# Optimization experiments

Measured on AMD Instinct MI355X. Metric: run time of the kernel, lower is better.

The kernel has to match this reference:

```python
import jax, jax.numpy as jnp
import numpy as np

D_MODEL = 512
D_ALPHA = 100
D_PH = 80
SCALE = 1.0 / np.sqrt(D_MODEL)


def gru_cell(x, h, Wih, Whh, bih, bhh):
    # PyTorch GRU gate order: r, z, n
    gi = x @ Wih.T + bih
    gh = h @ Whh.T + bhh
    ir, iz, inn = jnp.split(gi, 3, axis=-1)
    hr, hz, hn = jnp.split(gh, 3, axis=-1)
    r = jax.nn.sigmoid(ir + hr)
    z = jax.nn.sigmoid(iz + hz)
    n = jnp.tanh(inn + r * hn)
    return (1.0 - z) * n + z * h


def attend(q, k, v):
    # q: [B,D], k/v: [B,L,D]
    scores = jnp.einsum('bd,bld->bl', q, k) * SCALE
    a = jax.nn.softmax(scores, axis=-1)  # [B,L]
    o = jnp.einsum('bl,bld->bd', a, v)
    return a, o


def setup_inputs() -> dict:
    key = jax.random.key(0)
    ks = jax.random.split(key, 25)
    D = D_MODEL

    def u(k, shape, fan):
        return jax.random.uniform(k, shape, jnp.float32, -1.0, 1.0) / np.sqrt(fan)

    inp = {
        'text': jax.random.randint(ks[0], (256, 128), 0, D_ALPHA),
        'tgt': jax.random.randint(ks[1], (256, 64), 0, D_PH),
        'E_alpha': jax.random.normal(ks[2], (D_ALPHA, D), jnp.float32),
        'enc_Wih_f': u(ks[3], (3 * D, D), D),
        'enc_Whh_f': u(ks[4], (3 * D, D), D),
        'enc_bih_f': u(ks[5], (3 * D,), D),
        'enc_bhh_f': u(ks[6], (3 * D,), D),
        'enc_Wih_b': u(ks[7], (3 * D, D), D),
        'enc_Whh_b': u(ks[8], (3 * D, D), D),
        'enc_bih_b': u(ks[9], (3 * D,), D),
        'enc_bhh_b': u(ks[10], (3 * D,), D),
        'hpost_W': u(ks[11], (D, 2 * D), 2 * D),
        'hpost_b': u(ks[12], (D,), 2 * D),
        'wk_W': u(ks[13], (D, 2 * D), 2 * D),
        'wk_b': u(ks[14], (D,), 2 * D),
        'wv_W': u(ks[15], (D, 2 * D), 2 * D),
        'wv_b': u(ks[16], (D,), 2 * D),
        'E_ph': jax.random.normal(ks[17], (D_PH, D), jnp.float32),
        'dec_Wih': u(ks[18], (3 * D, 2 * D), 2 * D),
        'dec_Whh': u(ks[19], (3 * D, D), D),
        'dec_bih': u(ks[20], (3 * D,), D),
        'dec_bhh': u(ks[21], (3 * D,), D),
        'post_W': u(ks[22], (D_PH, D), D),
        'post_b': u(ks[23], (D_PH,), D),
    }
    return inp


def reference(text, tgt, E_alpha, enc_Wih_f, enc_Whh_f, enc_bih_f, enc_bhh_f,
              enc_Wih_b, enc_Whh_b, enc_bih_b, enc_bhh_b, hpost_W, hpost_b,
              wk_W, wk_b, wv_W, wv_b, E_ph, dec_Wih, dec_Whh, dec_bih,
              dec_bhh, post_W, post_b):
    B, LT = text.shape
    LP = tgt.shape[1]

    # ---- Encoder: bidirectional single-layer GRU (eval: dropout = identity)
    emb = E_alpha[text]                     # [B,LT,D]
    xs = jnp.swapaxes(emb, 0, 1)            # [LT,B,D]
    h0 = jnp.zeros((B, D_MODEL), emb.dtype)

    def mk_step(Wih, Whh, bih, bhh):
        def step(h, x):
            h2 = gru_cell(x, h, Wih, Whh, bih, bhh)
            return h2, h2
        return step

    hF, ysF = jax.lax.scan(mk_step(enc_Wih_f, enc_Whh_f, enc_bih_f, enc_bhh_f), h0, xs)
    hB, ysB = jax.lax.scan(mk_step(enc_Wih_b, enc_Whh_b, enc_bih_b, enc_bhh_b), h0, xs[::-1])
    ysB = ysB[::-1]
    enc_o = jnp.swapaxes(jnp.concatenate([ysF, ysB], axis=-1), 0, 1)  # [B,LT,2D]
    h = jnp.tanh(jnp.concatenate([hF, hB], axis=-1) @ hpost_W.T + hpost_b)  # [B,D]

    k = enc_o @ wk_W.T + wk_b               # [B,LT,D]
    v = enc_o @ wv_W.T + wv_b               # [B,LT,D]

    # ---- initial attention from encoder hidden; eval-mode first token is argmax
    # over tgt[:,0] reshaped to [B,1,1], i.e. always index 0.
    a_sl0, a_o0 = attend(h, k, v)
    dec_i0 = jnp.zeros((B,), jnp.int32)

    def dstep(carry, _):
        hh, a_o, a_sl, dec_i = carry
        e = E_ph[dec_i]                                  # [B,D]
        x = gru_cell(jnp.concatenate([e, a_o], axis=-1), hh,
                     dec_Wih, dec_Whh, dec_bih, dec_bhh)  # [B,D]
        o = x @ post_W.T + post_b                         # [B,D_PH]
        n_sl, n_o = attend(x, k, v)
        nxt = jnp.argmax(o, axis=-1).astype(jnp.int32)
        return (x, n_o, n_sl, nxt), (a_sl, o)

    _, (attn_t, res_t) = jax.lax.scan(dstep, (h, a_o0, a_sl0, dec_i0), None, length=LP)
    attn = jnp.swapaxes(attn_t, 0, 1)        # [B,LP,LT]
    res = jnp.swapaxes(res_t, 0, 1)          # [B,LP,D_PH]
    return attn, res
```

## Files before the change

### kernel.cpp

```cpp
#include <hip/hip_runtime.h>
#include <math.h>

#define B   256
#define LT  128
#define LP  64
#define DM  512
#define D3  1536
#define DPH 80
#define SCALE_F 0.044194173824159216f

__device__ __forceinline__ float dot4(float4 a, float4 b) {
    return a.x*b.x + a.y*b.y + a.z*b.z + a.w*b.w;
}
__device__ __forceinline__ float sigmoidf_(float x) {
    return 1.0f / (1.0f + expf(-x));
}

__device__ __forceinline__ void group_barrier(int* cnt, int target) {
    __syncthreads();
    if (threadIdx.x == 0) {
        __hip_atomic_fetch_add(cnt, 1, __ATOMIC_RELEASE,
                               __HIP_MEMORY_SCOPE_AGENT);
        while (__hip_atomic_load(cnt, __ATOMIC_RELAXED,
                                 __HIP_MEMORY_SCOPE_AGENT) < target)
            __builtin_amdgcn_s_sleep(16);
        __builtin_amdgcn_fence(__ATOMIC_ACQUIRE, "agent");
    }
    __syncthreads();
}

__global__ __launch_bounds__(256) void precompG_kernel(
    const float* __restrict__ Emb, const float* __restrict__ W,
    const float* __restrict__ bias, float* __restrict__ G,
    int wstride, int woff)
{
    const int n  = blockIdx.x * 256 + threadIdx.x;
    const int r0 = blockIdx.y * 4;
    __shared__ float es[4][DM];
    for (int i = threadIdx.x; i < 4 * DM; i += 256)
        es[i >> 9][i & 511] = Emb[(r0 + (i >> 9)) * DM + (i & 511)];
    __syncthreads();
    float acc[4] = {0.f, 0.f, 0.f, 0.f};
    const float* wr = &W[(size_t)n * wstride + woff];
    for (int j = 0; j < DM; j += 4) {
        float4 w4 = *(const float4*)&wr[j];
        #pragma unroll
        for (int rr = 0; rr < 4; ++rr) {
            float4 e4 = *(const float4*)&es[rr][j];
            acc[rr] += dot4(e4, w4);
        }
    }
    float bv = bias[n];
    #pragma unroll
    for (int rr = 0; rr < 4; ++rr)
        G[(r0 + rr) * D3 + n] = acc[rr] + bv;
}

__global__ __launch_bounds__(512, 1) void enc_persist_kernel(
    const float* __restrict__ Gf, const float* __restrict__ Gb,
    const float* __restrict__ Whh_f, const float* __restrict__ Whh_b,
    const float* __restrict__ bhh_f, const float* __restrict__ bhh_b,
    const int* __restrict__ text,
    float* __restrict__ hF0, float* __restrict__ hF1,
    float* __restrict__ hB0, float* __restrict__ hB1,
    float* __restrict__ E,
    const float* __restrict__ hpost_W, const float* __restrict__ hpost_b,
    float* __restrict__ hd0, int* __restrict__ bar)
{
    __shared__ float Wl[48][516];
    __shared__ float As[2][64][36];
    __shared__ float xs[1024];
    __shared__ float bl[48];

    const int tid  = threadIdx.x;
    const int blk  = blockIdx.x;
    const int dir  = blk & 1;
    const int bblk = (blk >> 1) & 3;
    const int jblk = blk >> 3;
    const int jtile = jblk * 16;
    const int btile = bblk * 64;
    int* cnt = bar + (blk & 7);

    const float* G   = dir ? Gb : Gf;
    const float* Whh = dir ? Whh_b : Whh_f;
    const float* bhh = dir ? bhh_b : bhh_f;
    float* h0 = dir ? hB0 : hF0;
    float* h1 = dir ? hB1 : hF1;
    const int yoff = dir ? DM : 0;

    for (int i = tid; i < 48 * 128; i += 512) {
        const int r = i >> 7, c = (i & 127) << 2;
        *(float4*)&Wl[r][c] =
            *(const float4*)&Whh[(size_t)((r >> 4) * DM + jtile + (r & 15)) * DM + c];
    }
    if (tid < 48) bl[tid] = bhh[(tid >> 4) * DM + jtile + (tid & 15)];
    __syncthreads();

    const int jj   = tid & 15;
    const int rg   = tid >> 4;
    const int lrow = tid >> 3;
    const int lcol = (tid & 7) * 4;

    for (int s = 0; s < LT; ++s) {
        const int t = dir ? (LT - 1 - s) : s;
        const float* hin = (s & 1) ? h1 : h0;
        float* hout      = (s & 1) ? h0 : h1;

        float acc[2][3];
        #pragma unroll
        for (int m = 0; m < 2; ++m) {
            acc[m][0] = 0.f; acc[m][1] = 0.f; acc[m][2] = 0.f;
        }

        float4 rA = *(const float4*)&hin[(btile + lrow) * DM + lcol];
        int buf = 0;
        for (int kc = 0; kc < 16; ++kc) {
            *(float4*)&As[buf][lrow][lcol] = rA;
            __syncthreads();
            if (kc < 15)
                rA = *(const float4*)&hin[(btile + lrow) * DM + (kc + 1) * 32 + lcol];
            const int kb = kc * 32;
            #pragma unroll
            for (int c4 = 0; c4 < 8; ++c4) {
                float4 bv0 = *(float4*)&Wl[jj][kb + c4 * 4];
                float4 bv1 = *(float4*)&Wl[16 + jj][kb + c4 * 4];
                float4 bv2 = *(float4*)&Wl[32 + jj][kb + c4 * 4];
                #pragma unroll
                for (int m = 0; m < 2; ++m) {
                    float4 av = *(float4*)&As[buf][rg * 2 + m][c4 * 4];
                    acc[m][0] += dot4(av, bv0);
                    acc[m][1] += dot4(av, bv1);
                    acc[m][2] += dot4(av, bv2);
                }
            }
            buf ^= 1;
            __syncthreads();
        }

        const int j = jtile + jj;
        #pragma unroll
        for (int m = 0; m < 2; ++m) {
            const int b = btile + rg * 2 + m;
            const int c = text[b * LT + t];
            float hr = acc[m][0] + bl[jj];
            float hz = acc[m][1] + bl[16 + jj];
            float hn = acc[m][2] + bl[32 + jj];
            float r = sigmoidf_(G[c * D3 + j] + hr);
            float z = sigmoidf_(G[c * D3 + DM + j] + hz);
            float n = tanhf(G[c * D3 + 2 * DM + j] + r * hn);
            float hp = hin[b * DM + j];
            float hv = (1.f - z) * n + z * hp;
            hout[b * DM + j] = hv;
            E[(size_t)(b * LT + t) * 1024 + yoff + j] = hv;
        }
        if (s < LT - 1) group_barrier(cnt, 32 * (s + 1));
    }

    group_barrier(bar + 8, 256);
    {
        const int b = blk;
        for (int i = tid; i < 1024; i += 512) {
            xs[i] = (i < DM) ? hF0[b * DM + i] : hB0[b * DM + (i - DM)];
        }
        __syncthreads();
        if (tid < DM) {
            const float* wr = &hpost_W[tid * 1024];
            float acc = 0.f;
            for (int jx = 0; jx < 1024; jx += 4)
                acc += dot4(*(const float4*)&xs[jx], *(const float4*)&wr[jx]);
            hd0[b * DM + tid] = tanhf(acc + hpost_b[tid]);
        }
    }
}

__global__ __launch_bounds__(256) void kv_chunk_kernel(
    const float* __restrict__ E,
    const float* __restrict__ wk, const float* __restrict__ wv,
    const float* __restrict__ kb, const float* __restrict__ vb,
    float* __restrict__ T, int r0)
{
    __shared__ float As[64][36];
    __shared__ float Bk[64][36];
    __shared__ float Bv[64][36];
    const int tid = threadIdx.x;
    const int nn = tid & 15, bb = tid >> 4;
    const int ntile = blockIdx.x * 64;
    const int mtile = blockIdx.y * 64;

    float ak[4][4], av_[4][4];
    #pragma unroll
    for (int m = 0; m < 4; ++m)
        #pragma unroll
        for (int i = 0; i < 4; ++i) { ak[m][i] = 0.f; av_[m][i] = 0.f; }

    const int lrow = tid >> 3;
    const int lcol = (tid & 7) * 4;

    for (int k0 = 0; k0 < 1024; k0 += 32) {
        __syncthreads();
        *(float4*)&As[lrow][lcol] =
            *(const float4*)&E[(size_t)(r0 + mtile + lrow) * 1024 + k0 + lcol];
        *(float4*)&As[lrow + 32][lcol] =
            *(const float4*)&E[(size_t)(r0 + mtile + lrow + 32) * 1024 + k0 + lcol];
        *(float4*)&Bk[lrow][lcol] =
            *(const float4*)&wk[(ntile + lrow) * 1024 + k0 + lcol];
        *(float4*)&Bk[lrow + 32][lcol] =
            *(const float4*)&wk[(ntile + lrow + 32) * 1024 + k0 + lcol];
        *(float4*)&Bv[lrow][lcol] =
            *(const float4*)&wv[(ntile + lrow) * 1024 + k0 + lcol];
        *(float4*)&Bv[lrow + 32][lcol] =
            *(const float4*)&wv[(ntile + lrow + 32) * 1024 + k0 + lcol];
        __syncthreads();
        #pragma unroll
        for (int c4 = 0; c4 < 8; ++c4) {
            float4 a4[4], k4[4], v4[4];
            #pragma unroll
            for (int m = 0; m < 4; ++m) a4[m] = *(float4*)&As[bb + 16 * m][c4 * 4];
            #pragma unroll
            for (int i = 0; i < 4; ++i) {
                k4[i] = *(float4*)&Bk[nn + 16 * i][c4 * 4];
                v4[i] = *(float4*)&Bv[nn + 16 * i][c4 * 4];
            }
            #pragma unroll
            for (int m = 0; m < 4; ++m)
                #pragma unroll
                for (int i = 0; i < 4; ++i) {
                    ak[m][i]  += dot4(a4[m], k4[i]);
                    av_[m][i] += dot4(a4[m], v4[i]);
                }
        }
    }
    #pragma unroll
    for (int m = 0; m < 4; ++m) {
        const int lm = mtile + bb + 16 * m;
        #pragma unroll
        for (int i = 0; i < 4; ++i) {
            const int gn = ntile + nn + 16 * i;
            T[(size_t)lm * 1024 + gn]       = ak[m][i]  + kb[gn];
            T[(size_t)lm * 1024 + DM + gn]  = av_[m][i] + vb[gn];
        }
    }
}

__global__ __launch_bounds__(256) void copy4_kernel(
    float4* __restrict__ dst, const float4* __restrict__ src, int n4)
{
    int i = blockIdx.x * 256 + threadIdx.x;
    const int stride = gridDim.x * 256;
    for (; i < n4; i += stride) dst[i] = src[i];
}

__device__ __forceinline__ void attend_body(
    int b, int tid, const float* __restrict__ q, const float* __restrict__ EKV,
    const float* __restrict__ post_W, const float* __restrict__ post_b,
    float* __restrict__ attn, float* __restrict__ res,
    float* __restrict__ a_o, int* __restrict__ dec_i,
    int s, int attn_row, int do_post, int do_attn,
    float* qs, float* part, float* sarr, float* red, float4 (*pvp)[128])
{
    if (tid < 128)
        *(float4*)&qs[tid * 4] = *(const float4*)&q[b * DM + tid * 4];
    __syncthreads();

    if (do_post) {
        if (tid < DPH) {
            const float* wr = &post_W[tid * DM];
            float acc = 0.f;
            for (int d = 0; d < DM; d += 4)
                acc += dot4(*(const float4*)&qs[d], *(const float4*)&wr[d]);
            float lv = acc + post_b[tid];
            res[(size_t)(b * LP + s) * DPH + tid] = lv;
            part[tid] = lv;
        }
        __syncthreads();
        if (tid == 0) {
            float best = part[0]; int bi = 0;
            for (int p = 1; p < DPH; ++p) {
                float vv = part[p];
                if (vv > best) { best = vv; bi = p; }
            }
            dec_i[b] = bi;
        }
        __syncthreads();
    }

    if (do_attn) {
        if (tid < 256) {
            const int r = tid & 127, half = tid >> 7;
            const float* kr = &EKV[(size_t)(b * LT + r) * 1024 + half * 256];
            const float* qh = &qs[half * 256];
            float p = 0.f;
            #pragma unroll
            for (int d = 0; d < 256; d += 4)
                p += dot4(*(const float4*)&qh[d], *(const float4*)&kr[d]);
            part[tid] = p;
        }
        __syncthreads();
        if (tid < LT) sarr[tid] = (part[tid] + part[tid + 128]) * SCALE_F;
        __syncthreads();
        if (tid < 64) {
            float m = fmaxf(sarr[tid], sarr[tid + 64]);
            #pragma unroll
            for (int off = 32; off > 0; off >>= 1)
                m = fmaxf(m, __shfl_xor(m, off));
            if (tid == 0) red[0] = m;
        }
        __syncthreads();
        const float smax = red[0];
        if (tid < LT) sarr[tid] = expf(sarr[tid] - smax);
        __syncthreads();
        if (tid < 64) {
            float ssum = sarr[tid] + sarr[tid + 64];
            #pragma unroll
            for (int off = 32; off > 0; off >>= 1)
                ssum += __shfl_xor(ssum, off);
            if (tid == 0) red[1] = ssum;
        }
        __syncthreads();
        const float inv = 1.0f / red[1];
        if (tid < LT) {
            float a = sarr[tid] * inv;
            sarr[tid] = a;
            attn[(size_t)(b * LP + attn_row) * LT + tid] = a;
        }
        __syncthreads();
        if (tid < 256) {
            const int d4 = tid & 127, half = tid >> 7;
            const float* vb0 = &EKV[(size_t)b * LT * 1024 + DM];
            float4 acc = make_float4(0.f, 0.f, 0.f, 0.f);
            const int l0 = half * 64;
            #pragma unroll 8
            for (int l = l0; l < l0 + 64; ++l) {
                float a = sarr[l];
                float4 v4 = *(const float4*)&vb0[(size_t)l * 1024 + d4 * 4];
                acc.x += a * v4.x; acc.y += a * v4.y;
                acc.z += a * v4.z; acc.w += a * v4.w;
            }
            pvp[half][d4] = acc;
        }
        __syncthreads();
        if (tid < 128) {
            float4 p0 = pvp[0][tid], p1 = pvp[1][tid];
            float4 o = make_float4(p0.x + p1.x, p0.y + p1.y,
                                   p0.z + p1.z, p0.w + p1.w);
            *(float4*)&a_o[b * DM + tid * 4] = o;
        }
    }
}

__global__ __launch_bounds__(512, 1) void dec_persist_kernel(
    const float* __restrict__ Gd,
    const float* __restrict__ dec_Wih, const float* __restrict__ dec_Whh,
    const float* __restrict__ dec_bhh,
    const float* __restrict__ EKV,
    const float* __restrict__ post_W, const float* __restrict__ post_b,
    float* __restrict__ attn, float* __restrict__ res,
    float* __restrict__ a_o, int* __restrict__ dec_i,
    float* __restrict__ hd0, float* __restrict__ hd1,
    int* __restrict__ bar)
{
    __shared__ float Wi[24][516];
    __shared__ float Wh[24][516];
    __shared__ float As[2][64][36];
    __shared__ float bl[24];
    __shared__ float qs[DM];
    __shared__ float part[256];
    __shared__ float sarr[LT];
    __shared__ float red[2];
    __shared__ float4 pvp[2][128];

    const int tid  = threadIdx.x;
    const int blk  = blockIdx.x;
    const int bblk = blk & 3;
    const int jblk = blk >> 2;
    const int jtile = jblk * 8;
    const int btile = bblk * 64;
    const int arow  = btile + jblk;
    int* cnt = bar + 9 + bblk;
    int nb = 0;

    for (int i = tid; i < 24 * 128; i += 512) {
        const int r = i >> 7, c = (i & 127) << 2;
        const int wrow = (r >> 3) * DM + jtile + (r & 7);
        *(float4*)&Wi[r][c] =
            *(const float4*)&dec_Wih[(size_t)wrow * 1024 + DM + c];
        *(float4*)&Wh[r][c] =
            *(const float4*)&dec_Whh[(size_t)wrow * DM + c];
    }
    if (tid < 24) bl[tid] = dec_bhh[(tid >> 3) * DM + jtile + (tid & 7)];
    __syncthreads();

    attend_body(arow, tid, hd0, EKV, post_W, post_b, attn, res, a_o, dec_i,
                0, 0, 0, 1, qs, part, sarr, red, pvp);
    ++nb; group_barrier(cnt, 64 * nb);

    const int jj   = tid & 7;
    const int rr   = tid >> 3;
    const int lrow = tid >> 3;
    const int lcol = (tid & 7) * 4;

    for (int s = 0; s < LP; ++s) {
        const float* hin = (s & 1) ? hd1 : hd0;
        float* hout      = (s & 1) ? hd0 : hd1;

        float acc[4] = {0.f, 0.f, 0.f, 0.f};

        #pragma unroll
        for (int ph = 0; ph < 2; ++ph) {
            const float* Aptr = (ph == 0) ? a_o : hin;
            const float (*W)[516] = (ph == 0) ? Wi : Wh;

            float4 rA = *(const float4*)&Aptr[(btile + lrow) * DM + lcol];
            int buf = 0;
            for (int kc = 0; kc < 16; ++kc) {
                *(float4*)&As[buf][lrow][lcol] = rA;
                __syncthreads();
                if (kc < 15)
                    rA = *(const float4*)&Aptr[(btile + lrow) * DM + (kc + 1) * 32 + lcol];
                const int kb = kc * 32;
                #pragma unroll
                for (int c4 = 0; c4 < 8; ++c4) {
                    float4 bv0 = *(float4*)&W[jj][kb + c4 * 4];
                    float4 bv1 = *(float4*)&W[8 + jj][kb + c4 * 4];
                    float4 bv2 = *(float4*)&W[16 + jj][kb + c4 * 4];
                    float4 av  = *(float4*)&As[buf][rr][c4 * 4];
                    acc[0]      += dot4(av, bv0);
                    acc[1]      += dot4(av, bv1);
                    acc[2 + ph] += dot4(av, bv2);
                }
                buf ^= 1;
                __syncthreads();
            }
        }

        {
            const int j = jtile + jj;
            const int b = btile + rr;
            const int c = dec_i[b];
            float r = sigmoidf_(Gd[c * D3 + j] + bl[jj] + acc[0]);
            float z = sigmoidf_(Gd[c * D3 + DM + j] + bl[8 + jj] + acc[1]);
            float n = tanhf(Gd[c * D3 + 2 * DM + j] + acc[2]
                            + r * (acc[3] + bl[16 + jj]));
            float hp = hin[b * DM + j];
            hout[b * DM + j] = (1.f - z) * n + z * hp;
        }
        ++nb; group_barrier(cnt, 64 * nb);

        attend_body(arow, tid, hout, EKV, post_W, post_b, attn, res, a_o, dec_i,
                    s, s + 1, 1, (s < LP - 1) ? 1 : 0,
                    qs, part, sarr, red, pvp);
        if (s < LP - 1) { ++nb; group_barrier(cnt, 64 * nb); }
    }
}

extern "C" void kernel_launch(void* const* d_in, const int* in_sizes, int n_in,
                              void* d_out, int out_size, void* d_ws, size_t ws_size,
                              hipStream_t stream)
{
    const int*   text    = (const int*)d_in[0];
    const float* E_alpha = (const float*)d_in[2];
    const float* Wih_f   = (const float*)d_in[3];
    const float* Whh_f   = (const float*)d_in[4];
    const float* bih_f   = (const float*)d_in[5];
    const float* bhh_f   = (const float*)d_in[6];
    const float* Wih_b   = (const float*)d_in[7];
    const float* Whh_b   = (const float*)d_in[8];
    const float* bih_b   = (const float*)d_in[9];
    const float* bhh_b   = (const float*)d_in[10];
    const float* hpost_W = (const float*)d_in[11];
    const float* hpost_b = (const float*)d_in[12];
    const float* wk_W    = (const float*)d_in[13];
    const float* wk_b    = (const float*)d_in[14];
    const float* wv_W    = (const float*)d_in[15];
    const float* wv_b    = (const float*)d_in[16];
    const float* E_ph    = (const float*)d_in[17];
    const float* dec_Wih = (const float*)d_in[18];
    const float* dec_Whh = (const float*)d_in[19];
    const float* dec_bih = (const float*)d_in[20];
    const float* dec_bhh = (const float*)d_in[21];
    const float* post_W  = (const float*)d_in[22];
    const float* post_b  = (const float*)d_in[23];

    float* ws = (float*)d_ws;
    float* Gf  = ws;
    float* Gb  = Gf  + 153600;
    float* Gd  = Gb  + 153600;
    float* hF0 = Gd  + 122880;
    float* hF1 = hF0 + 131072;
    float* hB0 = hF1 + 131072;
    float* hB1 = hB0 + 131072;
    float* hd0 = hB1 + 131072;
    float* hd1 = hd0 + 131072;
    float* a_o = hd1 + 131072;
    int*   dec_i = (int*)(a_o + 131072);
    int*   bar   = dec_i + 256;
    float* E   = a_o + 131072 + 512;
    float* T   = E + 33554432;

    hipMemsetAsync(hF0, 0, 131072 * sizeof(float), stream);
    hipMemsetAsync(hB0, 0, 131072 * sizeof(float), stream);
    hipMemsetAsync(dec_i, 0, (256 + 16) * sizeof(int), stream);

    precompG_kernel<<<dim3(6, 25), 256, 0, stream>>>(E_alpha, Wih_f, bih_f, Gf, DM, 0);
    precompG_kernel<<<dim3(6, 25), 256, 0, stream>>>(E_alpha, Wih_b, bih_b, Gb, DM, 0);
    precompG_kernel<<<dim3(6, 20), 256, 0, stream>>>(E_ph, dec_Wih, dec_bih, Gd, 1024, 0);

    enc_persist_kernel<<<dim3(256), 512, 0, stream>>>(
        Gf, Gb, Whh_f, Whh_b, bhh_f, bhh_b, text,
        hF0, hF1, hB0, hB1, E, hpost_W, hpost_b, hd0, bar);

    for (int c = 0; c < 2; ++c) {
        const int r0 = c * 16384;
        kv_chunk_kernel<<<dim3(8, 256), 256, 0, stream>>>(
            E, wk_W, wv_W, wk_b, wv_b, T, r0);
        copy4_kernel<<<dim3(4096), 256, 0, stream>>>(
            (float4*)(E + (size_t)r0 * 1024), (const float4*)T,
            16384 * 1024 / 4);
    }

    float* attn = (float*)d_out;
    float* res  = attn + (size_t)B * LP * LT;

    dec_persist_kernel<<<dim3(256), 512, 0, stream>>>(
        Gd, dec_Wih, dec_Whh, dec_bhh, E, post_W, post_b,
        attn, res, a_o, dec_i, hd0, hd1, bar);
}
```

Measured before the change: 11.92 ms.

## Replace acquire fences with cache-bypass loads and drop redundant tile barriers

Removes the agent-scope acquire fence from the group barrier and instead reads cross-block shared state (hidden states, attention outputs, decoder indices) with cache-bypassing sc0 sc1 global loads followed by explicit vmcnt waits. Drops the trailing __syncthreads in the double-buffered tile loops, relying on the ping-pong buffers to avoid overwrite hazards. Splits the attention score and PV reductions across all 512 threads in four quarters instead of 256 threads in halves. The risks are memory-ordering correctness without the acquire fence, and the inline asm waits serializing the loads.

```diff
diff --git a/kernel.cpp b/kernel.cpp
--- a/kernel.cpp
+++ b/kernel.cpp
@@ -14,6 +14,17 @@
 }
 __device__ __forceinline__ float sigmoidf_(float x) {
     return 1.0f / (1.0f + expf(-x));
+}
+
+__device__ __forceinline__ float4 issue_bypass4(const float* p) {
+    float4 v;
+    asm volatile("global_load_dwordx4 %0, %1, off sc0 sc1"
+                 : "=v"(v) : "v"(p));
+    return v;
+}
+__device__ __forceinline__ void wait_vm0() {
+    asm volatile("s_waitcnt vmcnt(0)" ::: "memory");
+    __builtin_amdgcn_sched_barrier(0);
 }
 
 __device__ __forceinline__ void group_barrier(int* cnt, int target) {
@@ -24,7 +35,6 @@
         while (__hip_atomic_load(cnt, __ATOMIC_RELAXED,
                                  __HIP_MEMORY_SCOPE_AGENT) < target)
             __builtin_amdgcn_s_sleep(16);
-        __builtin_amdgcn_fence(__ATOMIC_ACQUIRE, "agent");
     }
     __syncthreads();
 }
@@ -112,13 +122,15 @@
             acc[m][0] = 0.f; acc[m][1] = 0.f; acc[m][2] = 0.f;
         }
 
-        float4 rA = *(const float4*)&hin[(btile + lrow) * DM + lcol];
+        float4 rA = issue_bypass4(&hin[(btile + lrow) * DM + lcol]);
+        wait_vm0();
         int buf = 0;
         for (int kc = 0; kc < 16; ++kc) {
             *(float4*)&As[buf][lrow][lcol] = rA;
             __syncthreads();
+            float4 nA;
             if (kc < 15)
-                rA = *(const float4*)&hin[(btile + lrow) * DM + (kc + 1) * 32 + lcol];
+                nA = issue_bypass4(&hin[(btile + lrow) * DM + (kc + 1) * 32 + lcol]);
             const int kb = kc * 32;
             #pragma unroll
             for (int c4 = 0; c4 < 8; ++c4) {
@@ -133,8 +145,8 @@
                     acc[m][2] += dot4(av, bv2);
                 }
             }
+            if (kc < 15) { wait_vm0(); rA = nA; }
             buf ^= 1;
-            __syncthreads();
         }
 
         const int j = jtile + jj;
@@ -159,8 +171,12 @@
     group_barrier(bar + 8, 256);
     {
         const int b = blk;
-        for (int i = tid; i < 1024; i += 512) {
-            xs[i] = (i < DM) ? hF0[b * DM + i] : hB0[b * DM + (i - DM)];
+        if (tid < 256) {
+            float4 v = issue_bypass4((tid < 128)
+                ? &hF0[b * DM + tid * 4]
+                : &hB0[b * DM + (tid - 128) * 4]);
+            wait_vm0();
+            *(float4*)&xs[tid * 4] = v;
         }
         __syncthreads();
         if (tid < DM) {
@@ -258,8 +274,11 @@
     int s, int attn_row, int do_post, int do_attn,
     float* qs, float* part, float* sarr, float* red, float4 (*pvp)[128])
 {
-    if (tid < 128)
-        *(float4*)&qs[tid * 4] = *(const float4*)&q[b * DM + tid * 4];
+    if (tid < 128) {
+        float4 qv = issue_bypass4(&q[b * DM + tid * 4]);
+        wait_vm0();
+        *(float4*)&qs[tid * 4] = qv;
+    }
     __syncthreads();
 
     if (do_post) {
@@ -285,18 +304,22 @@
     }
 
     if (do_attn) {
-        if (tid < 256) {
-            const int r = tid & 127, half = tid >> 7;
-            const float* kr = &EKV[(size_t)(b * LT + r) * 1024 + half * 256];
-            const float* qh = &qs[half * 256];
-            float p = 0.f;
-            #pragma unroll
-            for (int d = 0; d < 256; d += 4)
-                p += dot4(*(const float4*)&qh[d], *(const float4*)&kr[d]);
-            part[tid] = p;
-        }
-        __syncthreads();
-        if (tid < LT) sarr[tid] = (part[tid] + part[tid + 128]) * SCALE_F;
+        {
+            const int r = tid & 127, quad = tid >> 7;
+            const float* kr = &EKV[(size_t)(b * LT + r) * 1024 + quad * 128];
+            const float* qh = &qs[quad * 128];
+            float p0 = 0.f, p1 = 0.f;
+            #pragma unroll
+            for (int d = 0; d < 128; d += 8) {
+                p0 += dot4(*(const float4*)&qh[d],     *(const float4*)&kr[d]);
+                p1 += dot4(*(const float4*)&qh[d + 4], *(const float4*)&kr[d + 4]);
+            }
+            part[tid] = p0 + p1;
+        }
+        __syncthreads();
+        if (tid < LT)
+            sarr[tid] = (((part[tid] + part[tid + 128]) + part[tid + 256])
+                         + part[tid + 384]) * SCALE_F;
         __syncthreads();
         if (tid < 64) {
             float m = fmaxf(sarr[tid], sarr[tid + 64]);
@@ -324,25 +347,33 @@
             attn[(size_t)(b * LP + attn_row) * LT + tid] = a;
         }
         __syncthreads();
-        if (tid < 256) {
-            const int d4 = tid & 127, half = tid >> 7;
+        {
+            const int d4 = tid & 127, quad = tid >> 7;
             const float* vb0 = &EKV[(size_t)b * LT * 1024 + DM];
-            float4 acc = make_float4(0.f, 0.f, 0.f, 0.f);
-            const int l0 = half * 64;
-            #pragma unroll 8
-            for (int l = l0; l < l0 + 64; ++l) {
-                float a = sarr[l];
-                float4 v4 = *(const float4*)&vb0[(size_t)l * 1024 + d4 * 4];
-                acc.x += a * v4.x; acc.y += a * v4.y;
-                acc.z += a * v4.z; acc.w += a * v4.w;
+            float4 a0 = make_float4(0.f, 0.f, 0.f, 0.f);
+            float4 a1 = make_float4(0.f, 0.f, 0.f, 0.f);
+            const int l0 = quad * 32;
+            #pragma unroll
+            for (int l = l0; l < l0 + 32; l += 2) {
+                float w0 = sarr[l], w1 = sarr[l + 1];
+                float4 v0 = *(const float4*)&vb0[(size_t)l * 1024 + d4 * 4];
+                float4 v1 = *(const float4*)&vb0[(size_t)(l + 1) * 1024 + d4 * 4];
+                a0.x += w0 * v0.x; a0.y += w0 * v0.y;
+                a0.z += w0 * v0.z; a0.w += w0 * v0.w;
+                a1.x += w1 * v1.x; a1.y += w1 * v1.y;
+                a1.z += w1 * v1.z; a1.w += w1 * v1.w;
             }
-            pvp[half][d4] = acc;
+            pvp[quad][d4] = make_float4(a0.x + a1.x, a0.y + a1.y,
+                                        a0.z + a1.z, a0.w + a1.w);
         }
         __syncthreads();
         if (tid < 128) {
             float4 p0 = pvp[0][tid], p1 = pvp[1][tid];
-            float4 o = make_float4(p0.x + p1.x, p0.y + p1.y,
-                                   p0.z + p1.z, p0.w + p1.w);
+            float4 p2 = pvp[2][tid], p3 = pvp[3][tid];
+            float4 o = make_float4(((p0.x + p1.x) + p2.x) + p3.x,
+                                   ((p0.y + p1.y) + p2.y) + p3.y,
+                                   ((p0.z + p1.z) + p2.z) + p3.z,
+                                   ((p0.w + p1.w) + p2.w) + p3.w);
             *(float4*)&a_o[b * DM + tid * 4] = o;
         }
     }
@@ -364,10 +395,10 @@
     __shared__ float As[2][64][36];
     __shared__ float bl[24];
     __shared__ float qs[DM];
-    __shared__ float part[256];
+    __shared__ float part[512];
     __shared__ float sarr[LT];
     __shared__ float red[2];
-    __shared__ float4 pvp[2][128];
+    __shared__ float4 pvp[4][128];
 
     const int tid  = threadIdx.x;
     const int blk  = blockIdx.x;
@@ -410,13 +441,15 @@
             const float* Aptr = (ph == 0) ? a_o : hin;
             const float (*W)[516] = (ph == 0) ? Wi : Wh;
 
-            float4 rA = *(const float4*)&Aptr[(btile + lrow) * DM + lcol];
-            int buf = 0;
+            float4 rA = issue_bypass4(&Aptr[(btile + lrow) * DM + lcol]);
+            wait_vm0();
+            int buf = (ph == 0) ? 0 : 0;
             for (int kc = 0; kc < 16; ++kc) {
                 *(float4*)&As[buf][lrow][lcol] = rA;
                 __syncthreads();
+                float4 nA;
                 if (kc < 15)
-                    rA = *(const float4*)&Aptr[(btile + lrow) * DM + (kc + 1) * 32 + lcol];
+                    nA = issue_bypass4(&Aptr[(btile + lrow) * DM + (kc + 1) * 32 + lcol]);
                 const int kb = kc * 32;
                 #pragma unroll
                 for (int c4 = 0; c4 < 8; ++c4) {
@@ -428,15 +461,17 @@
                     acc[1]      += dot4(av, bv1);
                     acc[2 + ph] += dot4(av, bv2);
                 }
+                if (kc < 15) { wait_vm0(); rA = nA; }
                 buf ^= 1;
-                __syncthreads();
             }
+            __syncthreads();
         }
 
         {
             const int j = jtile + jj;
             const int b = btile + rr;
-            const int c = dec_i[b];
+            const int c = __hip_atomic_load(&dec_i[b], __ATOMIC_RELAXED,
+                                            __HIP_MEMORY_SCOPE_SYSTEM);
             float r = sigmoidf_(Gd[c * D3 + j] + bl[jj] + acc[0]);
             float z = sigmoidf_(Gd[c * D3 + DM + j] + bl[8 + jj] + acc[1]);
             float n = tanhf(Gd[c * D3 + 2 * DM + j] + acc[2]
```

After: 12.03 ms. About the same (+1.0%).
